# Kernel optimization log

Measured on AMD Instinct MI355X. Metric: run time of the kernel, lower is better.

## Reference

```python
import jax, jax.numpy as jnp
import numpy as np

DIM = 512
NUM_HEADS = 8
HEAD_DIM = DIM // NUM_HEADS
SCALE = HEAD_DIM ** -0.5
HIDDEN = int(DIM * 4.0)
LN_EPS = 1e-5


def layer_norm(x, w, b):
    mu = jnp.mean(x, axis=-1, keepdims=True)
    var = jnp.var(x, axis=-1, keepdims=True)
    return (x - mu) * jax.lax.rsqrt(var + LN_EPS) * w + b


def setup_inputs() -> dict:
    key = jax.random.key(0)
    ks = jax.random.split(key, 8)
    s = 0.02
    return {
        "x": jax.random.normal(ks[0], (8, 4096, DIM), dtype=jnp.float32),
        "ln1_w": jnp.ones((DIM,), jnp.float32),
        "ln1_b": jnp.zeros((DIM,), jnp.float32),
        "qkv_w": jax.random.normal(ks[1], (3 * DIM, DIM), jnp.float32) * s,
        "proj_w": jax.random.normal(ks[2], (DIM, DIM), jnp.float32) * s,
        "proj_b": jnp.zeros((DIM,), jnp.float32),
        "ln2_w": jnp.ones((DIM,), jnp.float32),
        "ln2_b": jnp.zeros((DIM,), jnp.float32),
        "fc1_w": jax.random.normal(ks[3], (HIDDEN, DIM), jnp.float32) * s,
        "fc1_b": jnp.zeros((HIDDEN,), jnp.float32),
        "fc2_w": jax.random.normal(ks[4], (DIM, HIDDEN), jnp.float32) * s,
        "fc2_b": jnp.zeros((DIM,), jnp.float32),
        "eca_w": jax.random.normal(ks[5], (1, 1, 3), jnp.float32) * 0.5,
    }


def channel_attention(x, qkv_w, proj_w, proj_b):
    B, N, C = x.shape
    qkv = (x @ qkv_w.T).reshape(B, N, 3, NUM_HEADS, HEAD_DIM)
    qkv = qkv.transpose(2, 0, 3, 1, 4)  # (3, B, h, N, hd)
    q, k, v = qkv[0], qkv[1] * SCALE, qkv[2]
    # cross-covariance attention: (hd x hd) per head
    attn = jax.nn.softmax(jnp.einsum("bhnd,bhne->bhde", k, v), axis=-1)
    out = jnp.einsum("bhde,bhne->bhnd", attn, q)  # (B, h, N, hd)
    out = out.transpose(0, 2, 1, 3).reshape(B, N, C)
    return out @ proj_w.T + proj_b


def mlp_eca(x, fc1_w, fc1_b, fc2_w, fc2_b, eca_w):
    B, N, C = x.shape
    H = W = int(np.sqrt(N))
    h = jax.nn.gelu(x @ fc1_w.T + fc1_b, approximate=False)
    y = h @ fc2_w.T + fc2_b  # (B, N, C)
    # faithful replication of torch .view(B, C, H, W) on contiguous (B, N, C)
    y4 = y.reshape(B, C, H, W)
    pooled = jnp.mean(y4, axis=(2, 3))  # (B, C)
    conv = jax.lax.conv_general_dilated(
        pooled[:, None, :], eca_w, window_strides=(1,), padding=[(1, 1)],
        dimension_numbers=("NCW", "OIW", "NCW"))[:, 0, :]  # (B, C)
    gate = jax.nn.sigmoid(conv)[:, :, None, None]
    y4 = y4 * gate + y4
    return y4.reshape(B, C, H * W).transpose(0, 2, 1)  # (B, N, C)


def reference(x, ln1_w, ln1_b, qkv_w, proj_w, proj_b, ln2_w, ln2_b,
              fc1_w, fc1_b, fc2_w, fc2_b, eca_w):
    cur = layer_norm(x, ln1_w, ln1_b)
    x = x + channel_attention(cur, qkv_w, proj_w, proj_b)
    x = x + mlp_eca(layer_norm(x, ln2_w, ln2_b), fc1_w, fc1_b, fc2_w, fc2_b, eca_w)
    return x
```

## Files before the change

### kernel.cpp

```cpp
#include <hip/hip_runtime.h>
#include <hip/hip_bf16.h>

typedef __bf16 bf16;
typedef __bf16 bf16x8 __attribute__((ext_vector_type(8)));
typedef float floatx4 __attribute__((ext_vector_type(4)));

#define B_    8
#define N_    4096
#define C_    512
#define BN_   32768
#define HID_  2048
#define SCALE_ 0.125f

__device__ __forceinline__ void load_lds16(const void* g, void* l) {
    __builtin_amdgcn_global_load_lds(
        (const __attribute__((address_space(1))) void*)g,
        (__attribute__((address_space(3))) void*)l, 16, 0, 0);
}

__device__ __forceinline__ float gelu_fast(float v) {
    float c = fmaf(v * v, 0.044715f, 1.0f) * v;
    float e = __builtin_amdgcn_exp2f(-2.3022082f * c);
    return v * __builtin_amdgcn_rcpf(1.0f + e);
}

__global__ void sniff_kernel(const unsigned int* __restrict__ xw, int* __restrict__ flag)
{
    int t = threadIdx.x;
    int votes = 0;
#pragma unroll
    for (int i = 0; i < 4; i++) {
        unsigned w = xw[t * 4 + i];
        if (w == 0u) continue;
        unsigned a = w & 0xFFFFu;
        unsigned e = (a >> 7) & 0xFFu;
        if (a != 0u && e >= 110u && e <= 135u) votes++; else votes--;
    }
#pragma unroll
    for (int off = 32; off; off >>= 1) votes += __shfl_xor(votes, off);
    __shared__ int s[4];
    if ((t & 63) == 0) s[t >> 6] = votes;
    __syncthreads();
    if (t == 0) *flag = (s[0] + s[1] + s[2] + s[3]) > 0 ? 1 : 0;
}

struct ConvArgs {
    const void* src[12];
    unsigned    dstoff[12];
    int         n[12];
};

__global__ __launch_bounds__(256) void convert_params(
    ConvArgs args, char* __restrict__ ws, const int* __restrict__ flag)
{
    int seg = blockIdx.y;
    int n = args.n[seg];
    int base = blockIdx.x * 2048;
    if (base >= n) return;
    bf16* dst = (bf16*)(ws + args.dstoff[seg]);
    const void* src = args.src[seg];
    bool isbf = (*flag != 0);
#pragma unroll
    for (int j = 0; j < 8; j++) {
        int idx = base + threadIdx.x + j * 256;
        if (idx < n) {
            float v = isbf ? (float)((const bf16*)src)[idx]
                           : ((const float*)src)[idx];
            dst[idx] = (bf16)v;
        }
    }
}

__device__ __forceinline__ void ln_core(float f[8], const bf16* w, const bf16* b,
                                        int lane, bf16* outp)
{
    float s = 0.f, sq = 0.f;
#pragma unroll
    for (int j = 0; j < 8; j++) { s += f[j]; sq += f[j]*f[j]; }
#pragma unroll
    for (int off = 32; off; off >>= 1) { s += __shfl_xor(s, off); sq += __shfl_xor(sq, off); }
    float mean = s * (1.f/512.f);
    float var  = sq * (1.f/512.f) - mean*mean;
    float inv  = rsqrtf(var + 1e-5f);
    bf16x8 wv = *(const bf16x8*)(w + lane*8);
    bf16x8 bv = *(const bf16x8*)(b + lane*8);
    bf16x8 o;
#pragma unroll
    for (int j = 0; j < 8; j++) o[j] = (bf16)((f[j]-mean)*inv*(float)wv[j] + (float)bv[j]);
    *(bf16x8*)outp = o;
}

__global__ __launch_bounds__(256) void ln_dyn_kernel(
    const void* __restrict__ xv, const bf16* __restrict__ w,
    const bf16* __restrict__ b, bf16* __restrict__ out, const int* __restrict__ flag)
{
    int wave = threadIdx.x >> 6, lane = threadIdx.x & 63;
    size_t row = (size_t)blockIdx.x * 4 + wave;
    float f[8];
    if (*flag) {
        bf16x8 v = *(const bf16x8*)((const bf16*)xv + row * C_ + lane * 8);
#pragma unroll
        for (int j = 0; j < 8; j++) f[j] = (float)v[j];
    } else {
        const float4* p = (const float4*)((const float*)xv + row * C_ + lane * 8);
        float4 v0 = p[0], v1 = p[1];
        f[0]=v0.x; f[1]=v0.y; f[2]=v0.z; f[3]=v0.w;
        f[4]=v1.x; f[5]=v1.y; f[6]=v1.z; f[7]=v1.w;
    }
    ln_core(f, w, b, lane, out + row * C_ + lane*8);
}

__global__ __launch_bounds__(256) void ln_b16_kernel(
    const bf16* __restrict__ x, const bf16* __restrict__ w,
    const bf16* __restrict__ b, bf16* __restrict__ out)
{
    int wave = threadIdx.x >> 6, lane = threadIdx.x & 63;
    size_t row = (size_t)blockIdx.x * 4 + wave;
    bf16x8 v = *(const bf16x8*)(x + row * C_ + lane * 8);
    float f[8];
#pragma unroll
    for (int j = 0; j < 8; j++) f[j] = (float)v[j];
    ln_core(f, w, b, lane, out + row * C_ + lane*8);
}

__global__ __launch_bounds__(256) void ln_f32_kernel(
    const float* __restrict__ x, const bf16* __restrict__ w,
    const bf16* __restrict__ b, bf16* __restrict__ out)
{
    int wave = threadIdx.x >> 6, lane = threadIdx.x & 63;
    size_t row = (size_t)blockIdx.x * 4 + wave;
    const float4* p = (const float4*)(x + row * C_ + lane * 8);
    float4 v0 = p[0], v1 = p[1];
    float f[8] = { v0.x, v0.y, v0.z, v0.w, v1.x, v1.y, v1.z, v1.w };
    ln_core(f, w, b, lane, out + row * C_ + lane*8);
}

enum { EPI_NONE = 0, EPI_BIAS = 1, EPI_BIAS_RESID = 2, EPI_BIAS_GELU = 3, EPI_QKV = 4 };

__device__ __forceinline__ void stage_half(
    const bf16* __restrict__ G, int ldk, bf16* lbase, int t)
{
#pragma unroll
    for (int i = 0; i < 2; i++) {
        int c  = i * 512 + t;
        int r  = c >> 3;
        int ls = (c & 7) ^ (r & 7);
        load_lds16(G + (size_t)r * ldk + ls * 8, lbase + c * 8);
    }
}

#define LOAD_AF(half)                                                          \
    _Pragma("unroll") for (int mi = 0; mi < 4; mi++) {                         \
        int row = wm * 64 + mi * 16 + l16;                                     \
        _Pragma("unroll") for (int ks = 0; ks < 2; ks++)                       \
            af[mi][ks] = *(const bf16x8*)(&Asl[s][half][0][0] + row * 64 +     \
                ((ks * 32 + quad * 8) ^ ((row & 7) << 3)));                    \
    }
#define LOAD_BF(dst, half)                                                     \
    _Pragma("unroll") for (int ni = 0; ni < 2; ni++) {                         \
        int row = wn * 32 + ni * 16 + l16;                                     \
        _Pragma("unroll") for (int ks = 0; ks < 2; ks++)                       \
            dst[ni][ks] = *(const bf16x8*)(&Bsl[s][half][0][0] + row * 64 +    \
                ((ks * 32 + quad * 8) ^ ((row & 7) << 3)));                    \
    }
#define MFMA_Q(AH, BH, BFR)                                                    \
    __builtin_amdgcn_s_barrier();                                              \
    asm volatile("s_waitcnt lgkmcnt(0)");                                      \
    __builtin_amdgcn_s_setprio(1);                                             \
    _Pragma("unroll") for (int mi = 0; mi < 4; mi++)                           \
    _Pragma("unroll") for (int ni = 0; ni < 2; ni++)                           \
    _Pragma("unroll") for (int ks = 0; ks < 2; ks++)                           \
        acc[(AH)*4+mi][(BH)*2+ni] = __builtin_amdgcn_mfma_f32_16x16x32_bf16(   \
            af[mi][ks], BFR[ni][ks], acc[(AH)*4+mi][(BH)*2+ni], 0, 0, 0);      \
    __builtin_amdgcn_s_setprio(0);                                             \
    __builtin_amdgcn_s_barrier();

template<typename OutT, int EPI>
__global__ __launch_bounds__(512, 2) void gemm256(
    const bf16* __restrict__ A, const bf16* __restrict__ W,
    const bf16* __restrict__ bias, const void* __restrict__ resid,
    const int* __restrict__ flag,
    OutT* __restrict__ Cout, bf16* __restrict__ Cout2, int M, int Nn, int K)
{
    __shared__ bf16 Asl[2][2][128][64];
    __shared__ bf16 Bsl[2][2][128][64];
    const int t = threadIdx.x;
    const int wv = t >> 6, lane = t & 63;
    const int quad = lane >> 4, l16 = lane & 15;
    const int wm = wv >> 2, wn = wv & 3;
    const int Nt = Nn >> 8;
    const int total = (M >> 8) * Nt;
    const int G = gridDim.x;
    const int NKT = K >> 6;

    int id = blockIdx.x;
    if (id >= total) return;
    int m0 = (((id >> 3) / Nt) * 8 + (id & 7)) * 256;
    int n0 = ((id >> 3) % Nt) * 256;

    stage_half(A + (size_t)m0 * K,           K, &Asl[0][0][0][0], t);
    stage_half(W + (size_t)n0 * K,           K, &Bsl[0][0][0][0], t);
    stage_half(A + (size_t)(m0 + 128) * K,   K, &Asl[0][1][0][0], t);
    stage_half(W + (size_t)(n0 + 128) * K,   K, &Bsl[0][1][0][0], t);
    stage_half(A + (size_t)m0 * K + 64,      K, &Asl[1][0][0][0], t);
    stage_half(W + (size_t)n0 * K + 64,      K, &Bsl[1][0][0][0], t);
    asm volatile("s_waitcnt vmcnt(4)");
    __builtin_amdgcn_s_barrier();

    for (;;) {
        const int idn = id + G;
        const bool hn = idn < total;
        int m0n = 0, n0n = 0;
        if (hn) {
            m0n = (((idn >> 3) / Nt) * 8 + (idn & 7)) * 256;
            n0n = ((idn >> 3) % Nt) * 256;
        }

        floatx4 acc[8][4] = {};
        bf16x8 af[4][2], bf0[2][2], bf1[2][2];

        for (int kt = 0; kt < NKT; ++kt) {
            const int s = kt & 1;
            LOAD_AF(0)
            LOAD_BF(bf0, 0)
            {
                const bf16* p = (kt + 1 < NKT)
                    ? A + (size_t)(m0 + 128) * K + (size_t)(kt + 1) * 64
                    : (hn ? A + (size_t)(m0n + 128) * K : nullptr);
                if (p) stage_half(p, K, &Asl[s ^ 1][1][0][0], t);
            }
            MFMA_Q(0, 0, bf0)
            LOAD_BF(bf1, 1)
            {
                const bf16* p = (kt + 1 < NKT)
                    ? W + (size_t)(n0 + 128) * K + (size_t)(kt + 1) * 64
                    : (hn ? W + (size_t)(n0n + 128) * K : nullptr);
                if (p) stage_half(p, K, &Bsl[s ^ 1][1][0][0], t);
            }
            MFMA_Q(0, 1, bf1)
            LOAD_AF(1)
            {
                const bf16* p = (kt + 2 < NKT)
                    ? A + (size_t)m0 * K + (size_t)(kt + 2) * 64
                    : (hn ? A + (size_t)m0n * K + (size_t)(kt + 2 - NKT) * 64 : nullptr);
                if (p) stage_half(p, K, &Asl[s][0][0][0], t);
            }
            MFMA_Q(1, 1, bf1)
            {
                const bf16* p = (kt + 2 < NKT)
                    ? W + (size_t)n0 * K + (size_t)(kt + 2) * 64
                    : (hn ? W + (size_t)n0n * K + (size_t)(kt + 2 - NKT) * 64 : nullptr);
                if (p) stage_half(p, K, &Bsl[s][0][0][0], t);
            }
            if (kt + 1 < NKT || hn) {
                if (kt + 2 < NKT || hn) asm volatile("s_waitcnt vmcnt(4)");
                else                    asm volatile("s_waitcnt vmcnt(0)");
            }
            MFMA_Q(1, 0, bf0)
        }

        size_t ldc = (size_t)Nn; int csub = 0; bool to2 = false;
        if (EPI == EPI_QKV) {
            if (n0 >= 512) { to2 = true; ldc = 1024; csub = 512; }
            else           { ldc = 512; }
        }
        bool isbf = false;
        if (EPI == EPI_BIAS_RESID) isbf = (*flag != 0);

#pragma unroll
        for (int mg = 0; mg < 8; mg++) {
            int rowg = m0 + (mg >> 2) * 128 + wm * 64 + (mg & 3) * 16 + quad * 4;
#pragma unroll
            for (int ng = 0; ng < 4; ng++) {
                int col = n0 + (ng >> 1) * 128 + wn * 32 + (ng & 1) * 16 + l16;
                float bv = (EPI == EPI_BIAS || EPI == EPI_BIAS_RESID || EPI == EPI_BIAS_GELU)
                           ? (float)bias[col] : 0.f;
#pragma unroll
                for (int r = 0; r < 4; r++) {
                    size_t idx = (size_t)(rowg + r) * ldc + (col - csub);
                    float v = acc[mg][ng][r] + bv;
                    if (EPI == EPI_BIAS_RESID) {
                        float rres = isbf ? (float)((const bf16*)resid)[idx]
                                          : ((const float*)resid)[idx];
                        v += rres;
                    }
                    if (EPI == EPI_BIAS_GELU)  v = gelu_fast(v);
                    if (EPI == EPI_QKV && to2) Cout2[idx] = (bf16)v;
                    else                       Cout[idx]  = (OutT)v;
                }
            }
        }

        if (!hn) break;
        id = idn; m0 = m0n; n0 = n0n;
    }
}

__global__ __launch_bounds__(256) void attn_logits_mfma(
    const bf16* __restrict__ kv, float* __restrict__ partial)
{
    __shared__ bf16 Kt[64][136];
    __shared__ bf16 Vt[64][136];
    int s = blockIdx.x, bh = blockIdx.y, b = bh >> 3, h = bh & 7;
    int t = threadIdx.x, wave = t >> 6, lane = t & 63;
    int quad = lane >> 4, l16 = lane & 15;
    floatx4 acc[4] = {};
    for (int c = 0; c < 4; c++) {
        int n0 = s * 512 + c * 128;
        {
            int isv = t >> 7;
            int r   = t & 127;
            const bf16* gp = &kv[((size_t)b * N_ + n0 + r) * 1024 + h * 64 + isv * 512];
            bf16x8 rowv[8];
#pragma unroll
            for (int u = 0; u < 8; u++) rowv[u] = *(const bf16x8*)(gp + u * 8);
            bf16 (*dst)[136] = isv ? Vt : Kt;
#pragma unroll
            for (int u = 0; u < 8; u++)
#pragma unroll
                for (int jj = 0; jj < 8; jj++)
                    dst[u * 8 + jj][r] = rowv[u][jj];
        }
        __syncthreads();
#pragma unroll
        for (int ks = 0; ks < 4; ks++) {
            bf16x8 af = *(const bf16x8*)&Kt[wave * 16 + l16][ks * 32 + quad * 8];
#pragma unroll
            for (int ni = 0; ni < 4; ni++) {
                bf16x8 bfv = *(const bf16x8*)&Vt[ni * 16 + l16][ks * 32 + quad * 8];
                acc[ni] = __builtin_amdgcn_mfma_f32_16x16x32_bf16(af, bfv, acc[ni], 0, 0, 0);
            }
        }
        __syncthreads();
    }
    float* p = partial + ((size_t)bh * 8 + s) * 4096;
#pragma unroll
    for (int ni = 0; ni < 4; ni++)
#pragma unroll
        for (int r = 0; r < 4; r++)
            p[(wave * 16 + quad * 4 + r) * 64 + ni * 16 + l16] = acc[ni][r];
}

__global__ __launch_bounds__(256) void attn_softmax_kernel(
    const float* __restrict__ partial, bf16* __restrict__ attnb)
{
    int bh = blockIdx.y;
    int wave = threadIdx.x >> 6, lane = threadIdx.x & 63;
    for (int r = 0; r < 4; r++) {
        int d = blockIdx.x * 16 + wave * 4 + r;
        float v = 0.f;
#pragma unroll
        for (int s = 0; s < 8; s++) v += partial[((size_t)bh*8 + s)*4096 + d*64 + lane];
        v *= SCALE_;
        float m = v;
#pragma unroll
        for (int off = 32; off; off >>= 1) m = fmaxf(m, __shfl_xor(m, off));
        float p = expf(v - m);
        float sum = p;
#pragma unroll
        for (int off = 32; off; off >>= 1) sum += __shfl_xor(sum, off);
        attnb[(size_t)bh*4096 + d*64 + lane] = (bf16)(p / sum);
    }
}

__global__ __launch_bounds__(256) void attn_apply_mfma(
    const bf16* __restrict__ q, const bf16* __restrict__ attnb,
    bf16* __restrict__ outT)
{
    int bh = blockIdx.y, b = bh >> 3, h = bh & 7;
    int t = threadIdx.x, wave = t >> 6, lane = t & 63;
    int quad = lane >> 4, l16 = lane & 15;
    int nbase = blockIdx.x * 256 + wave * 64;
    bf16x8 bfrag[4][2];
#pragma unroll
    for (int di = 0; di < 4; di++)
#pragma unroll
        for (int ks = 0; ks < 2; ks++)
            bfrag[di][ks] = *(const bf16x8*)&attnb[(size_t)bh*4096 + (di*16 + l16)*64 + ks*32 + quad*8];
    floatx4 acc[4][4] = {};
#pragma unroll
    for (int mi = 0; mi < 4; mi++) {
#pragma unroll
        for (int ks = 0; ks < 2; ks++) {
            bf16x8 af = *(const bf16x8*)&q[((size_t)b*N_ + nbase + mi*16 + l16)*512 + h*64 + ks*32 + quad*8];
#pragma unroll
            for (int di = 0; di < 4; di++)
                acc[mi][di] = __builtin_amdgcn_mfma_f32_16x16x32_bf16(af, bfrag[di][ks], acc[mi][di], 0, 0, 0);
        }
    }
#pragma unroll
    for (int mi = 0; mi < 4; mi++)
#pragma unroll
        for (int di = 0; di < 4; di++)
#pragma unroll
            for (int r = 0; r < 4; r++)
                outT[((size_t)b*N_ + nbase + mi*16 + quad*4 + r)*512 + h*64 + di*16 + l16] =
                    (bf16)acc[mi][di][r];
}

__global__ __launch_bounds__(256) void pooled_kernel(
    const bf16* __restrict__ y, float* __restrict__ pooled)
{
    int bc = blockIdx.x;
    const bf16* p = y + (size_t)bc * 4096 + threadIdx.x * 16;
    float s = 0.f;
#pragma unroll
    for (int i = 0; i < 2; i++) {
        bf16x8 v = *(const bf16x8*)(p + i*8);
#pragma unroll
        for (int j = 0; j < 8; j++) s += (float)v[j];
    }
#pragma unroll
    for (int off = 32; off; off >>= 1) s += __shfl_xor(s, off);
    __shared__ float red[4];
    if ((threadIdx.x & 63) == 0) red[threadIdx.x >> 6] = s;
    __syncthreads();
    if (threadIdx.x == 0)
        pooled[bc] = (red[0] + red[1] + red[2] + red[3]) * (1.f/4096.f);
}

__global__ void gate_kernel(const float* __restrict__ pooled,
                            const bf16* __restrict__ eca_w, float* __restrict__ gate1)
{
    int c = threadIdx.x, b = blockIdx.x;
    float w0 = (float)eca_w[0], w1 = (float)eca_w[1], w2 = (float)eca_w[2];
    const float* p = pooled + b * 512;
    float conv = w1 * p[c];
    if (c > 0)   conv += w0 * p[c-1];
    if (c < 511) conv += w2 * p[c+1];
    float g = 1.f / (1.f + expf(-conv));
    gate1[b * 512 + c] = 1.f + g;
}

__global__ __launch_bounds__(256) void final_rmw(
    const bf16* __restrict__ y, const float* __restrict__ gate1,
    float* __restrict__ out)
{
    int b = blockIdx.z, c0 = blockIdx.y * 64, n0 = blockIdx.x * 64;
    __shared__ float ytile[64][65];
    int t = threadIdx.x;
#pragma unroll
    for (int i = 0; i < 2; i++) {
        int chunk = t * 2 + i;
        int ci = chunk >> 3, nj = (chunk & 7) * 8;
        bf16x8 v = *(const bf16x8*)&y[(size_t)b * ((size_t)N_*C_) + (size_t)(c0+ci) * 4096 + n0 + nj];
#pragma unroll
        for (int j = 0; j < 8; j++) ytile[ci][nj+j] = (float)v[j];
    }
    __syncthreads();
    int cc = t & 63, nb = t >> 6;
    float g = gate1[b * 512 + c0 + cc];
    for (int p = 0; p < 16; p++) {
        int nr = p * 4 + nb;
        size_t idx = ((size_t)b * N_ + n0 + nr) * C_ + c0 + cc;
        out[idx] = out[idx] + g * ytile[cc][nr];
    }
}

__global__ __launch_bounds__(256) void final_fresh(
    const bf16* __restrict__ y, const bf16* __restrict__ x2b,
    const float* __restrict__ gate1, float* __restrict__ out)
{
    int b = blockIdx.z, c0 = blockIdx.y * 64, n0 = blockIdx.x * 64;
    __shared__ float ytile[64][65];
    int t = threadIdx.x;
#pragma unroll
    for (int i = 0; i < 2; i++) {
        int chunk = t * 2 + i;
        int ci = chunk >> 3, nj = (chunk & 7) * 8;
        bf16x8 v = *(const bf16x8*)&y[(size_t)b * ((size_t)N_*C_) + (size_t)(c0+ci) * 4096 + n0 + nj];
#pragma unroll
        for (int j = 0; j < 8; j++) ytile[ci][nj+j] = (float)v[j];
    }
    __syncthreads();
    int cc = t & 63, nb = t >> 6;
    float g = gate1[b * 512 + c0 + cc];
    for (int p = 0; p < 16; p++) {
        int nr = p * 4 + nb;
        size_t idx = ((size_t)b * N_ + n0 + nr) * C_ + c0 + cc;
        out[idx] = (float)x2b[idx] + g * ytile[cc][nr];
    }
}

extern "C" void kernel_launch(void* const* d_in, const int* in_sizes, int n_in,
                              void* d_out, int out_size, void* d_ws, size_t ws_size,
                              hipStream_t stream)
{
    float* outf = (float*)d_out;
    bf16*  outb = (bf16*)d_out;
    char* ws = (char*)d_ws;

    int*   flag    = (int*)ws;
    float* pooled  = (float*)(ws + 4096);
    float* gate1   = (float*)(ws + 20480);
    bf16* ln1_w = (bf16*)(ws + 65536);
    bf16* ln1_b = (bf16*)(ws + 67584);
    bf16* ln2_w = (bf16*)(ws + 69632);
    bf16* ln2_b = (bf16*)(ws + 71680);
    bf16* proj_b= (bf16*)(ws + 73728);
    bf16* fc2_b = (bf16*)(ws + 75776);
    bf16* eca_w = (bf16*)(ws + 77824);
    bf16* fc1_b = (bf16*)(ws + 81920);
    bf16* qkv_w = (bf16*)(ws + ((size_t)1 << 20));
    bf16* proj_w= (bf16*)(ws + (size_t)2621440);
    bf16* fc1_w = (bf16*)(ws + ((size_t)3 << 20));
    bf16* fc2_w = (bf16*)(ws + ((size_t)5 << 20));
    float* partial = (float*)(ws + ((size_t)7  << 20));
    bf16*  attnb   = (bf16*)(ws + ((size_t)15 << 20));
    bf16*  T1      = (bf16*)(ws + ((size_t)16 << 20));
    bf16*  kvbuf   = (bf16*)(ws + ((size_t)48 << 20));
    bf16*  hbuf    = kvbuf;
    bf16*  x2b     = (bf16*)(ws + ((size_t)176 << 20));

    const bool fat = ws_size >= ((size_t)212 << 20);

    sniff_kernel<<<1, 256, 0, stream>>>((const unsigned int*)d_in[0], flag);

    ConvArgs ca;
    const int   srcidx[12] = { 1, 2, 6, 7, 5, 11, 12, 9, 3, 4, 8, 10 };
    const unsigned offs[12] = { 65536, 67584, 69632, 71680, 73728, 75776, 77824, 81920,
                                1u<<20, 2621440u, 3u<<20, 5u<<20 };
    for (int i = 0; i < 12; i++) {
        ca.src[i] = d_in[srcidx[i]];
        ca.dstoff[i] = offs[i];
        ca.n[i] = in_sizes[srcidx[i]];
    }
    convert_params<<<dim3(512, 12), 256, 0, stream>>>(ca, ws, flag);

    ln_dyn_kernel<<<BN_/4, 256, 0, stream>>>(d_in[0], ln1_w, ln1_b, T1, flag);

    gemm256<bf16, EPI_QKV><<<256, 512, 0, stream>>>(
        T1, qkv_w, nullptr, nullptr, flag, outb, kvbuf, BN_, 1536, 512);

    attn_logits_mfma<<<dim3(8, 64), 256, 0, stream>>>(kvbuf, partial);
    attn_softmax_kernel<<<dim3(4, 64), 256, 0, stream>>>(partial, attnb);
    attn_apply_mfma<<<dim3(16, 64), 256, 0, stream>>>(outb, attnb, T1);

    if (fat) {
        gemm256<bf16, EPI_BIAS_RESID><<<256, 512, 0, stream>>>(
            T1, proj_w, proj_b, d_in[0], flag, x2b, nullptr, BN_, 512, 512);
        ln_b16_kernel<<<BN_/4, 256, 0, stream>>>(x2b, ln2_w, ln2_b, T1);
        gemm256<bf16, EPI_BIAS_GELU><<<256, 512, 0, stream>>>(
            T1, fc1_w, fc1_b, nullptr, flag, hbuf, nullptr, BN_, 2048, 512);
        gemm256<bf16, EPI_BIAS><<<256, 512, 0, stream>>>(
            hbuf, fc2_w, fc2_b, nullptr, flag, T1, nullptr, BN_, 512, 2048);
        pooled_kernel<<<4096, 256, 0, stream>>>(T1, pooled);
        gate_kernel<<<8, 512, 0, stream>>>(pooled, eca_w, gate1);
        final_fresh<<<dim3(64, 8, 8), 256, 0, stream>>>(T1, x2b, gate1, outf);
    } else {
        gemm256<float, EPI_BIAS_RESID><<<256, 512, 0, stream>>>(
            T1, proj_w, proj_b, d_in[0], flag, outf, nullptr, BN_, 512, 512);
        ln_f32_kernel<<<BN_/4, 256, 0, stream>>>(outf, ln2_w, ln2_b, T1);
        for (int ch = 0; ch < 2; ch++) {
            bf16* Tch = T1 + (size_t)ch * 16384 * 512;
            gemm256<bf16, EPI_BIAS_GELU><<<256, 512, 0, stream>>>(
                Tch, fc1_w, fc1_b, nullptr, flag, hbuf, nullptr, 16384, 2048, 512);
            gemm256<bf16, EPI_BIAS><<<128, 512, 0, stream>>>(
                hbuf, fc2_w, fc2_b, nullptr, flag, Tch, nullptr, 16384, 512, 2048);
        }
        pooled_kernel<<<4096, 256, 0, stream>>>(T1, pooled);
        gate_kernel<<<8, 512, 0, stream>>>(pooled, eca_w, gate1);
        final_rmw<<<dim3(64, 8, 8), 256, 0, stream>>>(T1, gate1, outf);
    }
}
```

Measured before the change: 529.9 us.

## Software-pipeline LDS fragment reads with MFMA and precompute staging offsets

Restructures the GEMM main loop so LDS fragment reads for the next quadrant are issued before the current quadrant's MFMAs, with separate even/odd A fragment registers and a prefetch of the next tile's A fragment. Each stage now uses one barrier instead of two, and the per-thread global/LDS staging offsets are computed once outside the loop. The initial load order is also changed. The intent is to hide LDS latency behind matrix instructions and cut index arithmetic, at the cost of more live registers, which could raise spilling risk under the 512x2 launch bound.

```diff
diff --git a/kernel.cpp b/kernel.cpp
--- a/kernel.cpp
+++ b/kernel.cpp
@@ -137,43 +137,31 @@
 
 enum { EPI_NONE = 0, EPI_BIAS = 1, EPI_BIAS_RESID = 2, EPI_BIAS_GELU = 3, EPI_QKV = 4 };
 
-__device__ __forceinline__ void stage_half(
-    const bf16* __restrict__ G, int ldk, bf16* lbase, int t)
-{
-#pragma unroll
-    for (int i = 0; i < 2; i++) {
-        int c  = i * 512 + t;
-        int r  = c >> 3;
-        int ls = (c & 7) ^ (r & 7);
-        load_lds16(G + (size_t)r * ldk + ls * 8, lbase + c * 8);
-    }
-}
-
-#define LOAD_AF(half)                                                          \
+#define RD_A(dst, S, H)                                                        \
     _Pragma("unroll") for (int mi = 0; mi < 4; mi++) {                         \
         int row = wm * 64 + mi * 16 + l16;                                     \
         _Pragma("unroll") for (int ks = 0; ks < 2; ks++)                       \
-            af[mi][ks] = *(const bf16x8*)(&Asl[s][half][0][0] + row * 64 +     \
+            dst[mi][ks] = *(const bf16x8*)(&Asl[S][H][0][0] + row * 64 +       \
                 ((ks * 32 + quad * 8) ^ ((row & 7) << 3)));                    \
     }
-#define LOAD_BF(dst, half)                                                     \
+#define RD_B(dst, S, H)                                                        \
     _Pragma("unroll") for (int ni = 0; ni < 2; ni++) {                         \
         int row = wn * 32 + ni * 16 + l16;                                     \
         _Pragma("unroll") for (int ks = 0; ks < 2; ks++)                       \
-            dst[ni][ks] = *(const bf16x8*)(&Bsl[s][half][0][0] + row * 64 +    \
+            dst[ni][ks] = *(const bf16x8*)(&Bsl[S][H][0][0] + row * 64 +       \
                 ((ks * 32 + quad * 8) ^ ((row & 7) << 3)));                    \
     }
-#define MFMA_Q(AH, BH, BFR)                                                    \
-    __builtin_amdgcn_s_barrier();                                              \
-    asm volatile("s_waitcnt lgkmcnt(0)");                                      \
+#define MM(AF, BF, AH, BH)                                                     \
     __builtin_amdgcn_s_setprio(1);                                             \
     _Pragma("unroll") for (int mi = 0; mi < 4; mi++)                           \
     _Pragma("unroll") for (int ni = 0; ni < 2; ni++)                           \
     _Pragma("unroll") for (int ks = 0; ks < 2; ks++)                           \
         acc[(AH)*4+mi][(BH)*2+ni] = __builtin_amdgcn_mfma_f32_16x16x32_bf16(   \
-            af[mi][ks], BFR[ni][ks], acc[(AH)*4+mi][(BH)*2+ni], 0, 0, 0);      \
-    __builtin_amdgcn_s_setprio(0);                                             \
-    __builtin_amdgcn_s_barrier();
+            AF[mi][ks], BF[ni][ks], acc[(AH)*4+mi][(BH)*2+ni], 0, 0, 0);       \
+    __builtin_amdgcn_s_setprio(0);
+#define STAGE2(GB, LB)                                                         \
+    { load_lds16((GB) + goff0, (LB) + loff0);                                  \
+      load_lds16((GB) + goff1, (LB) + loff1); }
 
 template<typename OutT, int EPI>
 __global__ __launch_bounds__(512, 2) void gemm256(
@@ -193,19 +181,28 @@
     const int G = gridDim.x;
     const int NKT = K >> 6;
 
+    const int c0 = t, c1 = 512 + t;
+    const int r0 = c0 >> 3, r1 = c1 >> 3;
+    const size_t goff0 = (size_t)r0 * K + (size_t)(((c0 & 7) ^ (r0 & 7)) * 8);
+    const size_t goff1 = (size_t)r1 * K + (size_t)(((c1 & 7) ^ (r1 & 7)) * 8);
+    const int loff0 = c0 * 8, loff1 = c1 * 8;
+
     int id = blockIdx.x;
     if (id >= total) return;
     int m0 = (((id >> 3) / Nt) * 8 + (id & 7)) * 256;
     int n0 = ((id >> 3) % Nt) * 256;
 
-    stage_half(A + (size_t)m0 * K,           K, &Asl[0][0][0][0], t);
-    stage_half(W + (size_t)n0 * K,           K, &Bsl[0][0][0][0], t);
-    stage_half(A + (size_t)(m0 + 128) * K,   K, &Asl[0][1][0][0], t);
-    stage_half(W + (size_t)(n0 + 128) * K,   K, &Bsl[0][1][0][0], t);
-    stage_half(A + (size_t)m0 * K + 64,      K, &Asl[1][0][0][0], t);
-    stage_half(W + (size_t)n0 * K + 64,      K, &Bsl[1][0][0][0], t);
+    STAGE2(A + (size_t)m0 * K,         &Asl[0][0][0][0]);
+    STAGE2(W + (size_t)n0 * K,         &Bsl[0][0][0][0]);
+    STAGE2(A + (size_t)(m0 + 128) * K, &Asl[0][1][0][0]);
+    STAGE2(W + (size_t)n0 * K + 64,    &Bsl[1][0][0][0]);
+    STAGE2(W + (size_t)(n0 + 128) * K, &Bsl[0][1][0][0]);
+    STAGE2(A + (size_t)m0 * K + 64,    &Asl[1][0][0][0]);
     asm volatile("s_waitcnt vmcnt(4)");
     __builtin_amdgcn_s_barrier();
+
+    bf16x8 afE[4][2], afO[4][2], bf0[2][2], bf1[2][2];
+    RD_A(afE, 0, 0)
 
     for (;;) {
         const int idn = id + G;
@@ -217,46 +214,52 @@
         }
 
         floatx4 acc[8][4] = {};
-        bf16x8 af[4][2], bf0[2][2], bf1[2][2];
 
         for (int kt = 0; kt < NKT; ++kt) {
             const int s = kt & 1;
-            LOAD_AF(0)
-            LOAD_BF(bf0, 0)
             {
                 const bf16* p = (kt + 1 < NKT)
                     ? A + (size_t)(m0 + 128) * K + (size_t)(kt + 1) * 64
                     : (hn ? A + (size_t)(m0n + 128) * K : nullptr);
-                if (p) stage_half(p, K, &Asl[s ^ 1][1][0][0], t);
-            }
-            MFMA_Q(0, 0, bf0)
-            LOAD_BF(bf1, 1)
+                if (p) STAGE2(p, &Asl[s ^ 1][1][0][0]);
+            }
+            __builtin_amdgcn_s_barrier();
+            RD_B(bf0, s, 0)
+            RD_B(bf1, s, 1)
+            __builtin_amdgcn_sched_barrier(0);
+            MM(afE, bf0, 0, 0)
             {
                 const bf16* p = (kt + 1 < NKT)
                     ? W + (size_t)(n0 + 128) * K + (size_t)(kt + 1) * 64
                     : (hn ? W + (size_t)(n0n + 128) * K : nullptr);
-                if (p) stage_half(p, K, &Bsl[s ^ 1][1][0][0], t);
-            }
-            MFMA_Q(0, 1, bf1)
-            LOAD_AF(1)
+                if (p) STAGE2(p, &Bsl[s ^ 1][1][0][0]);
+            }
+            __builtin_amdgcn_s_barrier();
+            RD_A(afO, s, 1)
+            __builtin_amdgcn_sched_barrier(0);
+            MM(afE, bf1, 0, 1)
             {
                 const bf16* p = (kt + 2 < NKT)
                     ? A + (size_t)m0 * K + (size_t)(kt + 2) * 64
                     : (hn ? A + (size_t)m0n * K + (size_t)(kt + 2 - NKT) * 64 : nullptr);
-                if (p) stage_half(p, K, &Asl[s][0][0][0], t);
-            }
-            MFMA_Q(1, 1, bf1)
+                if (p) STAGE2(p, &Asl[s][0][0][0]);
+            }
+            __builtin_amdgcn_s_barrier();
+            MM(afO, bf1, 1, 1)
             {
                 const bf16* p = (kt + 2 < NKT)
                     ? W + (size_t)n0 * K + (size_t)(kt + 2) * 64
                     : (hn ? W + (size_t)n0n * K + (size_t)(kt + 2 - NKT) * 64 : nullptr);
-                if (p) stage_half(p, K, &Bsl[s][0][0][0], t);
+                if (p) STAGE2(p, &Bsl[s][0][0][0]);
             }
             if (kt + 1 < NKT || hn) {
                 if (kt + 2 < NKT || hn) asm volatile("s_waitcnt vmcnt(4)");
                 else                    asm volatile("s_waitcnt vmcnt(0)");
             }
-            MFMA_Q(1, 0, bf0)
+            __builtin_amdgcn_s_barrier();
+            if (kt + 1 < NKT || hn) { RD_A(afE, s ^ 1, 0) }
+            __builtin_amdgcn_sched_barrier(0);
+            MM(afO, bf0, 1, 0)
         }
 
         size_t ldc = (size_t)Nn; int csub = 0; bool to2 = false;
```

Measured after the change: 538.1 us. Within noise of the previous version (+1.6%).
